# Optimization experiments

Measured on AMD Instinct MI355X. Metric: run time of the kernel, lower is better.

The kernel has to match this reference:

```python
import jax, jax.numpy as jnp
import numpy as np

# ---- static config (from init_kwargs) ----
SAMPLE_RATE = 2048.0
MAX_SHIFT = int(0.025 * SAMPLE_RATE)          # 51 samples
NUM_BINS = 16
FFTLENGTH = 1.0                               # chisq_kernel_length (s)
DF = 1.0 / FFTLENGTH
NUM_FREQS = int(FFTLENGTH * SAMPLE_RATE // 2 + 1)   # 1025 == rfft bins of 2048 samples
HIGHPASS = 32.0
CHISQ_PENALTY = 1.0
_freqs = np.arange(NUM_FREQS) / FFTLENGTH
MASK = _freqs >= HIGHPASS                     # static numpy bool mask

BATCH, CHANNELS, DIM = 256, 2, 2048


def setup_inputs() -> dict:
    key = jax.random.key(0)
    k1, k2 = jax.random.split(key)
    x_hat = jax.random.normal(k1, (BATCH, CHANNELS, DIM), dtype=jnp.float32)
    x = jax.random.normal(k2, (BATCH, CHANNELS, DIM), dtype=jnp.float32)
    return {"x_hat": x_hat, "x": x}


def _center(x):
    xmin = x.min(-1, keepdims=True)
    xmax = x.max(-1, keepdims=True)
    return 2 * (x - xmin) / (xmax - xmin) - 1


def _shifted_pearson(x, y, max_shift):
    # x, y: [B, C, T]; returns corr: [W, B, C] with W = 2*max_shift + 1
    b, c, t = x.shape
    num_windows = 2 * max_shift + 1
    xp = jnp.pad(x, ((0, 0), (0, 0), (max_shift, max_shift)))
    # window w, position i -> xp[..., i + w]  (same layout as torch unfold)
    idx = jnp.arange(num_windows)[:, None] + jnp.arange(t)[None, :]   # [W, T]
    xw = xp[:, :, idx]                                                # [B, C, W, T]
    xw = jnp.transpose(xw, (2, 0, 1, 3))                              # [W, B, C, T]
    xw = xw - xw.mean(-1, keepdims=True)
    yc = y - y.mean(-1, keepdims=True)
    corr = (xw * yc).sum(-1)
    norm = (xw ** 2).sum(-1) * (yc ** 2).sum(-1)
    return corr / jnp.sqrt(norm)


def _snr_integral(a, b):
    # |4 * a * conj(b) * df| cumulatively summed over frequency
    integrand = a * jnp.conj(b)
    return jnp.abs(4 * integrand * DF).cumsum(-1)


def _chisq(htilde, stilde):
    htilde = htilde[:, :, MASK]
    stilde = stilde[:, :, MASK]
    # partition frequencies by the template's own optimal-SNR integral
    si = _snr_integral(htilde, htilde)                    # [B, C, F]
    total = si[:, :, -1:]
    bins = (jnp.arange(NUM_BINS + 1, dtype=si.dtype) / NUM_BINS) * total  # [B, C, NB+1]
    search = jax.vmap(jax.vmap(lambda a, v: jnp.searchsorted(a, v, side="right")))
    edges = search(si, bins)
    edges = jnp.clip(edges, 0, si.shape[-1] - 1)
    qtilde = htilde / jnp.sqrt(total).astype(htilde.dtype)
    # SNR per bin of the normalized template against the strain
    si2 = _snr_integral(qtilde, stilde)                   # [B, C, F]
    total2 = si2[:, :, -1:]
    right = jnp.take_along_axis(si2, edges[:, :, 1:], axis=-1)
    left = jnp.take_along_axis(si2, edges[:, :, :-1], axis=-1)
    snr_per_bin = right - left                            # [B, C, NB]
    summand = (snr_per_bin - total2 / NUM_BINS) ** 2
    chisq = NUM_BINS * summand.sum(-1) / (NUM_BINS - 1)
    return total2[:, :, 0], chisq


def reference(x_hat, x):
    x_hat = _center(x_hat)
    corr = _shifted_pearson(x_hat, x, MAX_SHIFT)          # [W, B, C]
    corr = corr.max(0)                                    # [B, C]
    loss = (1 - corr) / (1 + corr)
    htilde = jnp.fft.rfft(x_hat, axis=-1) / SAMPLE_RATE   # [B, C, 1025] complex
    stilde = jnp.fft.rfft(x, axis=-1) / SAMPLE_RATE
    _, chisq = _chisq(htilde, stilde)
    chisq = chisq * CHISQ_PENALTY
    loss = loss * (1 + chisq ** 3) ** (1.0 / 6.0)
    return loss
```

## Files before the change

### kernel.cpp

```cpp
#include <hip/hip_runtime.h>
#include <math.h>

#define ROWS 512
#define DIM 2048
#define MS 51
#define NWIN 103
#define KMIN 32
#define NMASK 993
#define PHYS(i) ((i) + ((i) >> 5))

__global__ __launch_bounds__(512) void fused_mfl_kernel(
    const float* __restrict__ xhat, const float* __restrict__ x,
    float* __restrict__ out)
{
    const int r = blockIdx.x;
    const int t = threadIdx.x;
    const int lane = t & 63;
    const int wave = t >> 6;
    const float* xh = xhat + (size_t)r * DIM;
    const float* xr = x + (size_t)r * DIM;

    __shared__ float smem[9216];
    float* yh    = smem;
    float* yc    = smem + 2224;
    float* headS = smem + 4352;
    float* headQ = smem + 4404;
    float* tailS = smem + 4456;
    float* tailQ = smem + 4508;
    float2* A  = (float2*)smem;
    float2* Bb = (float2*)(smem + 4096);
    float2* TW = (float2*)(smem + 8192);
    float* siA  = smem;
    float* siBr = smem + 1024;

    __shared__ float red[32];
    __shared__ float sc[8];
    __shared__ int   edges[17];
    __shared__ float summ[16];
    __shared__ float wsA[8], wsB[8];

    float4 a4 = ((const float4*)xh)[t];
    float4 b4 = ((const float4*)xr)[t];
    float av[4] = {a4.x, a4.y, a4.z, a4.w};
    float bv[4] = {b4.x, b4.y, b4.z, b4.w};

    {
        float swv, cwv;
        sincosf((float)t * (-3.14159265358979323846f / 1024.0f), &swv, &cwv);
        TW[t] = make_float2(cwv, swv);
    }

    float mn = av[0], mx = av[0], sx = 0.f;
#pragma unroll
    for (int j = 0; j < 4; ++j) {
        mn = fminf(mn, av[j]); mx = fmaxf(mx, av[j]); sx += bv[j];
    }
#pragma unroll
    for (int d = 32; d; d >>= 1) {
        mn = fminf(mn, __shfl_down(mn, d));
        mx = fmaxf(mx, __shfl_down(mx, d));
        sx += __shfl_down(sx, d);
    }
    if (lane == 0) { red[wave] = mn; red[8 + wave] = mx; red[16 + wave] = sx; }
    __syncthreads();
    if (t == 0) {
        float m0 = red[0], m1 = red[8], s = red[16];
        for (int w = 1; w < 8; ++w) {
            m0 = fminf(m0, red[w]); m1 = fmaxf(m1, red[8 + w]); s += red[16 + w];
        }
        sc[0] = m0; sc[1] = m1; sc[2] = s * (1.0f / DIM);
    }
    __syncthreads();
    mn = sc[0]; mx = sc[1];
    const float mean = sc[2];
    const float scale = 2.0f / (mx - mn);

    float s1 = 0.f, s2 = 0.f, syy = 0.f;
    float yhv[4];
#pragma unroll
    for (int j = 0; j < 4; ++j) {
        float y = (av[j] - mn) * scale - 1.0f;
        float z = bv[j] - mean;
        yhv[j] = y;
        s1 += y; s2 += y * y; syy += z * z;
        int i = 4 * t + j;
        yh[PHYS(i + MS)] = y;
        yc[PHYS(i)] = z;
    }
    if (t < MS) { yh[PHYS(t)] = 0.f; yh[PHYS(t + MS + DIM)] = 0.f; }

#pragma unroll
    for (int d = 32; d; d >>= 1) {
        s1 += __shfl_down(s1, d); s2 += __shfl_down(s2, d); syy += __shfl_down(syy, d);
    }
    if (lane == 0) { red[wave] = s1; red[8 + wave] = s2; red[16 + wave] = syy; }
    __syncthreads();
    if (t == 0) {
        float p0 = 0.f, p1 = 0.f, p2 = 0.f;
        for (int w = 0; w < 8; ++w) { p0 += red[w]; p1 += red[8 + w]; p2 += red[16 + w]; }
        sc[3] = p0; sc[4] = p1; sc[5] = p2;
    }
    __syncthreads();
    const float S1 = sc[3], S2 = sc[4], Syy = sc[5];

    if (wave < 2) {
        float v = 0.f;
        if (lane >= 1 && lane <= MS)
            v = (wave == 0) ? yh[PHYS(MS + lane - 1)] : yh[PHYS(MS + DIM - lane)];
        float s = v, q = v * v;
#pragma unroll
        for (int d = 1; d < 64; d <<= 1) {
            float ys = __shfl_up(s, d);
            float yq = __shfl_up(q, d);
            if (lane >= d) { s += ys; q += yq; }
        }
        if (lane <= MS) {
            if (wave == 0) { headS[lane] = s; headQ[lane] = q; }
            else           { tailS[lane] = s; tailQ[lane] = q; }
        }
    }
    __syncthreads();

    float ycr[32];
#pragma unroll
    for (int j = 0; j < 32; ++j) ycr[j] = yc[PHYS(32 * lane + j)];

    const int c0 = 13 * wave;
    const int base0 = 32 * lane + c0;
    float wreg[32];
#pragma unroll
    for (int j = 0; j < 32; ++j) wreg[j] = yh[PHYS(base0 + j)];

    float cmax = -2.0f;
#pragma unroll
    for (int i = 0; i < 13; ++i) {
        float acc = 0.f;
#pragma unroll
        for (int j = 0; j < 32; ++j) acc += wreg[(i + j) & 31] * ycr[j];
#pragma unroll
        for (int d = 32; d; d >>= 1) acc += __shfl_down(acc, d);
        int c = c0 + i;
        if (lane == 0 && c < NWIN) {
            int off = c - MS;
            float sw, qw;
            if (off >= 0) { sw = S1 - headS[off]; qw = S2 - headQ[off]; }
            else          { sw = S1 - tailS[-off]; qw = S2 - tailQ[-off]; }
            float varw = qw - sw * sw * (1.0f / DIM);
            float corr = acc / sqrtf(varw * Syy);
            cmax = fmaxf(cmax, corr);
        }
        if (i < 12) wreg[i & 31] = yh[PHYS(base0 + 32 + i)];
    }
    if (lane == 0) red[wave] = cmax;
    __syncthreads();
    if (t == 0) {
        float m = red[0];
        for (int w = 1; w < 8; ++w) m = fmaxf(m, red[w]);
        sc[6] = (1.0f - m) / (1.0f + m);
    }

#pragma unroll
    for (int j = 0; j < 4; ++j) {
        A[4 * t + j] = make_float2(yhv[j], bv[j]);
    }
    __syncthreads();

    float2 *S = A, *D = Bb;
#pragma unroll
    for (int stage = 0; stage < 5; ++stage) {
        const int s = 1 << (2 * stage);
        const int q = t;
        const int u = q & ~(s - 1);
        float2 x0 = S[q];
        float2 x1 = S[q + 512];
        float2 x2 = S[q + 1024];
        float2 x3 = S[q + 1536];
        float t0r = x0.x + x2.x, t0i = x0.y + x2.y;
        float t1r = x0.x - x2.x, t1i = x0.y - x2.y;
        float t2r = x1.x + x3.x, t2i = x1.y + x3.y;
        float d3r = x1.x - x3.x, d3i = x1.y - x3.y;
        float t3r = d3i, t3i = -d3r;
        float2 w1 = TW[u];
        float w2r = w1.x * w1.x - w1.y * w1.y, w2i = 2.f * w1.x * w1.y;
        float w3r = w2r * w1.x - w2i * w1.y,  w3i = w2r * w1.y + w2i * w1.x;
        float y0r = t0r + t2r, y0i = t0i + t2i;
        float a1r = t1r + t3r, a1i = t1i + t3i;
        float y1r = a1r * w1.x - a1i * w1.y, y1i = a1r * w1.y + a1i * w1.x;
        float a2r = t0r - t2r, a2i = t0i - t2i;
        float y2r = a2r * w2r - a2i * w2i, y2i = a2r * w2i + a2i * w2r;
        float a3r = t1r - t3r, a3i = t1i - t3i;
        float y3r = a3r * w3r - a3i * w3i, y3i = a3r * w3i + a3i * w3r;
        int base = q + 3 * u;
        D[base]         = make_float2(y0r, y0i);
        D[base + s]     = make_float2(y1r, y1i);
        D[base + 2 * s] = make_float2(y2r, y2i);
        D[base + 3 * s] = make_float2(y3r, y3i);
        __syncthreads();
        float2* tmp = S; S = D; D = tmp;
    }

    const float MSC = 0.5f * (1.0f / 2048.0f);
    float h[2], sg[2];
#pragma unroll
    for (int j = 0; j < 2; ++j) {
        int m = 2 * t + j;
        if (m < NMASK) {
            int f = m + KMIN;
            float zfr, zfi;
            if (f < 1024) {
                float2 p = S[f], q2 = S[f + 1024];
                zfr = p.x + q2.x; zfi = p.y + q2.y;
            } else {
                float2 p = S[0], q2 = S[1024];
                zfr = p.x - q2.x; zfi = p.y - q2.y;
            }
            int g = 2048 - f;
            float2 p2 = S[g - 1024], q3 = S[g];
            float zgr = p2.x - q3.x, zgi = p2.y - q3.y;
            float hre = zfr + zgr, him = zfi - zgi;
            float sre = zfi + zgi, sim = zgr - zfr;
            h[j]  = sqrtf(hre * hre + him * him) * MSC;
            sg[j] = sqrtf(sre * sre + sim * sim) * MSC;
        } else { h[j] = 0.f; sg[j] = 0.f; }
    }

    float e0 = 4.f * h[0] * h[0];
    float e1 = e0 + 4.f * h[1] * h[1];
    float g0 = 4.f * h[0] * sg[0];
    float g1 = g0 + 4.f * h[1] * sg[1];
    float totE = e1, totG = g1;
    float incE = totE, incG = totG;
#pragma unroll
    for (int d = 1; d < 64; d <<= 1) {
        float yE = __shfl_up(incE, d);
        float yG = __shfl_up(incG, d);
        if (lane >= d) { incE += yE; incG += yG; }
    }
    if (lane == 63) { wsA[wave] = incE; wsB[wave] = incG; }
    __syncthreads();
    float offE = 0.f, offG = 0.f;
    for (int w = 0; w < wave; ++w) { offE += wsA[w]; offG += wsB[w]; }
    float preE = offE + incE - totE;
    float preG = offG + incG - totG;
    siA[2 * t]      = preE + e0;
    siA[2 * t + 1]  = preE + e1;
    siBr[2 * t]     = preG + g0;
    siBr[2 * t + 1] = preG + g1;
    __syncthreads();
    const float total  = siA[NMASK - 1];
    const float qf     = 1.0f / sqrtf(total);
    const float total2 = siBr[NMASK - 1] * qf;

    if (t < 17) {
        float bin = ((float)t * (1.0f / 16.0f)) * total;
        int lo = 0, hi = NMASK;
        while (lo < hi) {
            int mid = (lo + hi) >> 1;
            if (siA[mid] <= bin) lo = mid + 1; else hi = mid;
        }
        edges[t] = (lo < NMASK - 1) ? lo : (NMASK - 1);
    }
    __syncthreads();

    if (t < 16) {
        float snr = (siBr[edges[t + 1]] - siBr[edges[t]]) * qf;
        float d = snr - total2 * (1.0f / 16.0f);
        summ[t] = d * d;
    }
    __syncthreads();
    if (t == 0) {
        float ssum = 0.f;
        for (int i = 0; i < 16; ++i) ssum += summ[i];
        float chisq = 16.0f * ssum / 15.0f;
        float c3 = chisq * chisq * chisq;
        out[r] = sc[6] * powf(1.0f + c3, 1.0f / 6.0f);
    }
}

extern "C" void kernel_launch(void* const* d_in, const int* in_sizes, int n_in,
                              void* d_out, int out_size, void* d_ws, size_t ws_size,
                              hipStream_t stream) {
    const float* xhat = (const float*)d_in[0];
    const float* x    = (const float*)d_in[1];
    float* out = (float*)d_out;
    (void)d_ws; (void)ws_size;

    fused_mfl_kernel<<<ROWS, 512, 0, stream>>>(xhat, x, out);
}
```

Before: 73.22 us.

## Merge centering and moment reductions into one pass and batch correlation reductions via LDS

The min/max/sum reduction and the second-moment reduction are merged into a single LDS-staged pass. The centered sums S1, S2 and Syy are now derived algebraically from raw moments, which removes two barriers and one reduction round. The shifted-correlation loop no longer does a 6-step wave shuffle reduction per window. Instead it writes partial sums to LDS and reduces all 103 windows in parallel across threads. This uses more shared memory (64KB), which may limit occupancy, and computing variance from raw moments carries some risk of cancellation.

```diff
diff --git a/kernel.cpp b/kernel.cpp
--- a/kernel.cpp
+++ b/kernel.cpp
@@ -20,20 +20,22 @@
     const float* xh = xhat + (size_t)r * DIM;
     const float* xr = x + (size_t)r * DIM;
 
-    __shared__ float smem[9216];
+    __shared__ float smem[16384];
+    float* red6  = smem;
     float* yh    = smem;
     float* yc    = smem + 2224;
     float* headS = smem + 4352;
     float* headQ = smem + 4404;
     float* tailS = smem + 4456;
     float* tailQ = smem + 4508;
+    float* V     = smem + 9216;
+    float* corrv = smem + 16220;
     float2* A  = (float2*)smem;
     float2* Bb = (float2*)(smem + 4096);
     float2* TW = (float2*)(smem + 8192);
     float* siA  = smem;
     float* siBr = smem + 1024;
 
-    __shared__ float red[32];
     __shared__ float sc[8];
     __shared__ int   edges[17];
     __shared__ float summ[16];
@@ -50,58 +52,75 @@
         TW[t] = make_float2(cwv, swv);
     }
 
-    float mn = av[0], mx = av[0], sx = 0.f;
+    {
+        float mn4 = fminf(fminf(av[0], av[1]), fminf(av[2], av[3]));
+        float mx4 = fmaxf(fmaxf(av[0], av[1]), fmaxf(av[2], av[3]));
+        float sa = (av[0] + av[1]) + (av[2] + av[3]);
+        float qa = (av[0]*av[0] + av[1]*av[1]) + (av[2]*av[2] + av[3]*av[3]);
+        float sx = (bv[0] + bv[1]) + (bv[2] + bv[3]);
+        float qx = (bv[0]*bv[0] + bv[1]*bv[1]) + (bv[2]*bv[2] + bv[3]*bv[3]);
+        red6[t]        = mn4;
+        red6[512 + t]  = mx4;
+        red6[1024 + t] = sa;
+        red6[1536 + t] = qa;
+        red6[2048 + t] = sx;
+        red6[2560 + t] = qx;
+    }
+    __syncthreads();
+    if (wave == 0) {
+        float4 u, v;
+        u = ((const float4*)(red6       ))[2*lane]; v = ((const float4*)(red6       ))[2*lane+1];
+        float pmn = fminf(fminf(fminf(u.x,u.y),fminf(u.z,u.w)),
+                          fminf(fminf(v.x,v.y),fminf(v.z,v.w)));
+        u = ((const float4*)(red6 +  512))[2*lane]; v = ((const float4*)(red6 +  512))[2*lane+1];
+        float pmx = fmaxf(fmaxf(fmaxf(u.x,u.y),fmaxf(u.z,u.w)),
+                          fmaxf(fmaxf(v.x,v.y),fmaxf(v.z,v.w)));
+        u = ((const float4*)(red6 + 1024))[2*lane]; v = ((const float4*)(red6 + 1024))[2*lane+1];
+        float psa = ((u.x+u.y)+(u.z+u.w)) + ((v.x+v.y)+(v.z+v.w));
+        u = ((const float4*)(red6 + 1536))[2*lane]; v = ((const float4*)(red6 + 1536))[2*lane+1];
+        float pqa = ((u.x+u.y)+(u.z+u.w)) + ((v.x+v.y)+(v.z+v.w));
+        u = ((const float4*)(red6 + 2048))[2*lane]; v = ((const float4*)(red6 + 2048))[2*lane+1];
+        float psx = ((u.x+u.y)+(u.z+u.w)) + ((v.x+v.y)+(v.z+v.w));
+        u = ((const float4*)(red6 + 2560))[2*lane]; v = ((const float4*)(red6 + 2560))[2*lane+1];
+        float pqx = ((u.x+u.y)+(u.z+u.w)) + ((v.x+v.y)+(v.z+v.w));
+#pragma unroll
+        for (int d = 32; d; d >>= 1) {
+            pmn = fminf(pmn, __shfl_down(pmn, d));
+            pmx = fmaxf(pmx, __shfl_down(pmx, d));
+            psa += __shfl_down(psa, d);
+            pqa += __shfl_down(pqa, d);
+            psx += __shfl_down(psx, d);
+            pqx += __shfl_down(pqx, d);
+        }
+        if (lane == 0) {
+            float mn = pmn, mx = pmx;
+            float scl = 2.0f / (mx - mn);
+            float mean = psx * (1.0f / DIM);
+            float Sm = psa - (float)DIM * mn;
+            float S1 = scl * Sm - (float)DIM;
+            float S2 = scl * scl * (pqa - 2.f * mn * psa + (float)DIM * mn * mn)
+                     - 2.f * scl * Sm + (float)DIM;
+            float Syy = pqx - (float)DIM * mean * mean;
+            sc[0] = mn; sc[1] = scl; sc[2] = mean;
+            sc[3] = S1; sc[4] = S2; sc[5] = Syy;
+        }
+    }
+    __syncthreads();
+    const float mnv = sc[0], scl = sc[1], mean = sc[2];
+    const float S1 = sc[3], S2 = sc[4], Syy = sc[5];
+
+    float yhv[4];
 #pragma unroll
     for (int j = 0; j < 4; ++j) {
-        mn = fminf(mn, av[j]); mx = fmaxf(mx, av[j]); sx += bv[j];
-    }
-#pragma unroll
-    for (int d = 32; d; d >>= 1) {
-        mn = fminf(mn, __shfl_down(mn, d));
-        mx = fmaxf(mx, __shfl_down(mx, d));
-        sx += __shfl_down(sx, d);
-    }
-    if (lane == 0) { red[wave] = mn; red[8 + wave] = mx; red[16 + wave] = sx; }
-    __syncthreads();
-    if (t == 0) {
-        float m0 = red[0], m1 = red[8], s = red[16];
-        for (int w = 1; w < 8; ++w) {
-            m0 = fminf(m0, red[w]); m1 = fmaxf(m1, red[8 + w]); s += red[16 + w];
-        }
-        sc[0] = m0; sc[1] = m1; sc[2] = s * (1.0f / DIM);
-    }
-    __syncthreads();
-    mn = sc[0]; mx = sc[1];
-    const float mean = sc[2];
-    const float scale = 2.0f / (mx - mn);
-
-    float s1 = 0.f, s2 = 0.f, syy = 0.f;
-    float yhv[4];
-#pragma unroll
-    for (int j = 0; j < 4; ++j) {
-        float y = (av[j] - mn) * scale - 1.0f;
+        float y = (av[j] - mnv) * scl - 1.0f;
         float z = bv[j] - mean;
         yhv[j] = y;
-        s1 += y; s2 += y * y; syy += z * z;
         int i = 4 * t + j;
         yh[PHYS(i + MS)] = y;
         yc[PHYS(i)] = z;
     }
     if (t < MS) { yh[PHYS(t)] = 0.f; yh[PHYS(t + MS + DIM)] = 0.f; }
-
-#pragma unroll
-    for (int d = 32; d; d >>= 1) {
-        s1 += __shfl_down(s1, d); s2 += __shfl_down(s2, d); syy += __shfl_down(syy, d);
-    }
-    if (lane == 0) { red[wave] = s1; red[8 + wave] = s2; red[16 + wave] = syy; }
-    __syncthreads();
-    if (t == 0) {
-        float p0 = 0.f, p1 = 0.f, p2 = 0.f;
-        for (int w = 0; w < 8; ++w) { p0 += red[w]; p1 += red[8 + w]; p2 += red[16 + w]; }
-        sc[3] = p0; sc[4] = p1; sc[5] = p2;
-    }
-    __syncthreads();
-    const float S1 = sc[3], S2 = sc[4], Syy = sc[5];
+    __syncthreads();
 
     if (wave < 2) {
         float v = 0.f;
@@ -119,7 +138,6 @@
             else           { tailS[lane] = s; tailQ[lane] = q; }
         }
     }
-    __syncthreads();
 
     float ycr[32];
 #pragma unroll
@@ -131,39 +149,50 @@
 #pragma unroll
     for (int j = 0; j < 32; ++j) wreg[j] = yh[PHYS(base0 + j)];
 
-    float cmax = -2.0f;
+    float pacc[13];
 #pragma unroll
     for (int i = 0; i < 13; ++i) {
         float acc = 0.f;
 #pragma unroll
         for (int j = 0; j < 32; ++j) acc += wreg[(i + j) & 31] * ycr[j];
-#pragma unroll
-        for (int d = 32; d; d >>= 1) acc += __shfl_down(acc, d);
+        pacc[i] = acc;
+        if (i < 12) wreg[i & 31] = yh[PHYS(base0 + 32 + i)];
+    }
+#pragma unroll
+    for (int i = 0; i < 13; ++i) {
         int c = c0 + i;
-        if (lane == 0 && c < NWIN) {
+        if (c < NWIN) V[68 * c + lane] = pacc[i];
+    }
+    __syncthreads();
+
+    if (t < 4 * NWIN) {
+        int c = t >> 2, k = t & 3;
+        const float4* vp = (const float4*)(V + 68 * c + 16 * k);
+        float4 u0 = vp[0], u1 = vp[1], u2 = vp[2], u3 = vp[3];
+        float acc = ((u0.x+u0.y)+(u0.z+u0.w)) + ((u1.x+u1.y)+(u1.z+u1.w))
+                  + ((u2.x+u2.y)+(u2.z+u2.w)) + ((u3.x+u3.y)+(u3.z+u3.w));
+        acc += __shfl_down(acc, 1);
+        acc += __shfl_down(acc, 2);
+        if (k == 0) {
             int off = c - MS;
             float sw, qw;
             if (off >= 0) { sw = S1 - headS[off]; qw = S2 - headQ[off]; }
             else          { sw = S1 - tailS[-off]; qw = S2 - tailQ[-off]; }
             float varw = qw - sw * sw * (1.0f / DIM);
-            float corr = acc / sqrtf(varw * Syy);
-            cmax = fmaxf(cmax, corr);
-        }
-        if (i < 12) wreg[i & 31] = yh[PHYS(base0 + 32 + i)];
-    }
-    if (lane == 0) red[wave] = cmax;
-    __syncthreads();
-    if (t == 0) {
-        float m = red[0];
-        for (int w = 1; w < 8; ++w) m = fmaxf(m, red[w]);
-        sc[6] = (1.0f - m) / (1.0f + m);
-    }
-
-#pragma unroll
-    for (int j = 0; j < 4; ++j) {
-        A[4 * t + j] = make_float2(yhv[j], bv[j]);
-    }
-    __syncthreads();
+            corrv[c] = acc / sqrtf(varw * Syy);
+        }
+    }
+#pragma unroll
+    for (int j = 0; j < 4; ++j) A[4 * t + j] = make_float2(yhv[j], bv[j]);
+    __syncthreads();
+
+    if (wave == 0) {
+        float m = (lane < NWIN) ? corrv[lane] : -2.0f;
+        if (lane + 64 < NWIN) m = fmaxf(m, corrv[lane + 64]);
+#pragma unroll
+        for (int d = 32; d; d >>= 1) m = fmaxf(m, __shfl_down(m, d));
+        if (lane == 0) sc[6] = (1.0f - m) / (1.0f + m);
+    }
 
     float2 *S = A, *D = Bb;
 #pragma unroll
@@ -283,7 +312,7 @@
     const float* xhat = (const float*)d_in[0];
     const float* x    = (const float*)d_in[1];
     float* out = (float*)d_out;
-    (void)d_ws; (void)ws_size;
+    (void)in_sizes; (void)n_in; (void)out_size; (void)d_ws; (void)ws_size;
 
     fused_mfl_kernel<<<ROWS, 512, 0, stream>>>(xhat, x, out);
 }
```

Result: faster. 69.95 us (-4.5%).
